# Optimization experiments

Measured on AMD Instinct MI355X. Metric: run time of the kernel, lower is better.

The kernel has to match this reference:

```python
import jax, jax.numpy as jnp
import numpy as np

A = 81          # agents / zones (9x9 grid)
DMAX = 5        # max neighborhood size (self + 4-neighbors)
NGLOB = 48      # global obs block width
HID = 128
B = 16384
LN_EPS = 1e-12  # tf.contrib.layers.layer_norm epsilon
BN_EPS = 1e-3   # tf.contrib.layers.batch_norm epsilon
NEG = -1e30


def _grid_adjacency():
    side = 9
    idx = np.zeros((A, DMAX), np.int32)
    mask = np.zeros((A, DMAX), bool)
    for i in range(A):
        r, c = divmod(i, side)
        nb = [i]
        for dr, dc in ((-1, 0), (1, 0), (0, -1), (0, 1)):
            rr, cc = r + dr, c + dc
            if 0 <= rr < side and 0 <= cc < side:
                nb.append(rr * side + cc)
        idx[i, :len(nb)] = nb
        mask[i, :len(nb)] = True
    return jnp.asarray(idx), jnp.asarray(mask)


def setup_inputs() -> dict:
    key = jax.random.key(0)
    ks = jax.random.split(key, 8)
    neigh_idx, neigh_mask = _grid_adjacency()
    in_dim = 2 * DMAX + NGLOB  # padded local obs width (58)
    s = 0.05
    return {
        "obs": jax.random.normal(ks[0], (B, 210), jnp.float32),
        "neigh_idx": neigh_idx,
        "neigh_mask": neigh_mask,
        "W1": jax.random.normal(ks[1], (A, in_dim, HID), jnp.float32) * s,
        "b1": jnp.zeros((A, HID), jnp.float32),
        "ln1_g": jnp.ones((A, HID), jnp.float32),
        "ln1_b": jnp.zeros((A, HID), jnp.float32),
        "bn1_b": jnp.zeros((A, HID), jnp.float32),
        "W2": jax.random.normal(ks[2], (A, HID, HID), jnp.float32) * s,
        "b2": jnp.zeros((A, HID), jnp.float32),
        "ln2_g": jnp.ones((A, HID), jnp.float32),
        "ln2_b": jnp.zeros((A, HID), jnp.float32),
        "bn2_b": jnp.zeros((A, HID), jnp.float32),
        "Wout": jax.random.normal(ks[3], (A, HID, DMAX), jnp.float32) * s,
        "bout": jnp.zeros((A, DMAX), jnp.float32),
    }


def _layer_norm(x, g, b):
    mu = jnp.mean(x, axis=-1, keepdims=True)
    var = jnp.mean(jnp.square(x - mu), axis=-1, keepdims=True)
    return (x - mu) * jax.lax.rsqrt(var + LN_EPS) * g[:, None, :] + b[:, None, :]


def _batch_norm(x, beta):
    # training-mode batch norm over the batch axis (axis=1), center only (scale=False)
    mu = jnp.mean(x, axis=1, keepdims=True)
    var = jnp.mean(jnp.square(x - mu), axis=1, keepdims=True)
    return (x - mu) * jax.lax.rsqrt(var + BN_EPS) + beta[:, None, :]


def reference(obs, neigh_idx, neigh_mask, W1, b1, ln1_g, ln1_b, bn1_b,
              W2, b2, ln2_g, ln2_b, bn2_b, Wout, bout):
    m = neigh_mask[:, None, :].astype(obs.dtype)          # [A,1,DMAX]
    g1 = obs[:, NGLOB + neigh_idx].transpose(1, 0, 2)      # [A,B,DMAX] zone block 1
    g2 = obs[:, NGLOB + 81 + neigh_idx].transpose(1, 0, 2)  # [A,B,DMAX] zone block 2
    glob = jnp.broadcast_to(obs[None, :, :NGLOB], (A, obs.shape[0], NGLOB))
    x = jnp.concatenate([g1 * m, g2 * m, glob], axis=-1)   # [A,B,58] (padded slots zeroed)

    h = jnp.einsum('abi,aio->abo', x, W1) + b1[:, None, :]
    h = jax.nn.relu(_batch_norm(_layer_norm(h, ln1_g, ln1_b), bn1_b))
    h = jnp.einsum('abi,aio->abo', h, W2) + b2[:, None, :]
    h = jax.nn.relu(_batch_norm(_layer_norm(h, ln2_g, ln2_b), bn2_b))

    logits = jnp.einsum('abi,aid->abd', h, Wout) + bout[:, None, :]  # [A,B,DMAX]
    logits = jnp.where(neigh_mask[:, None, :], logits, NEG)
    p = jax.nn.softmax(logits, axis=-1) * m                # masked softmax over valid neighbors

    oh = jax.nn.one_hot(neigh_idx, A, dtype=p.dtype)       # [A,DMAX,81] scatter map
    out = jnp.einsum('abd,adn->abn', p, oh)                # scatter into fixed 81-vector
    return out.transpose(1, 0, 2)                          # [B,A,81]
```

## Files before the change

kernel.cpp:

```cpp
#include <hip/hip_runtime.h>
#include <stdint.h>
#include <stddef.h>

#define N_AG 81
#define HID 128
#define TROWS 128

typedef __bf16 bf16x8 __attribute__((ext_vector_type(8)));
typedef float f32x4 __attribute__((ext_vector_type(4)));
typedef uint32_t u32v4 __attribute__((ext_vector_type(4)));
typedef uint32_t u32v2 __attribute__((ext_vector_type(2)));

#define PB1 0
#define PLG1 128
#define PLB1 256
#define PBN1 384
#define PMU1 512
#define PRS1 640
#define PB2 768
#define PLG2 896
#define PLB2 1024
#define PBN2 1152
#define PMU2 1280
#define PRS2 1408

__device__ __forceinline__ unsigned short f2bf(float f) {
  uint32_t u = __builtin_bit_cast(uint32_t, f);
  u += 0x7fffu + ((u >> 16) & 1u);
  return (unsigned short)(u >> 16);
}

__device__ __forceinline__ f32x4 f4z() { f32x4 v; v[0]=0.f; v[1]=0.f; v[2]=0.f; v[3]=0.f; return v; }

__device__ __forceinline__ bf16x8 ld_frag(const uint8_t* p) {
  u32v4 v = *(const u32v4*)p;
  return __builtin_bit_cast(bf16x8, v);
}

__device__ __forceinline__ f32x4 mfma16(bf16x8 a, bf16x8 b, f32x4 c) {
  return __builtin_amdgcn_mfma_f32_16x16x32_bf16(a, b, c, 0, 0, 0);
}

__device__ __forceinline__ void bias_ln(f32x4 (&acc)[8][2], const float* s_par,
                                        int PB, int PG, int PBb, int g) {
  #pragma unroll
  for (int mf = 0; mf < 8; ++mf) {
    #pragma unroll
    for (int rg = 0; rg < 4; ++rg) {
      float bo = s_par[PB + 16 * mf + 4 * g + rg];
      acc[mf][0][rg] += bo;
      acc[mf][1][rg] += bo;
    }
  }
  #pragma unroll
  for (int nf = 0; nf < 2; ++nf) {
    float s = 0.f;
    #pragma unroll
    for (int mf = 0; mf < 8; ++mf) {
      #pragma unroll
      for (int rg = 0; rg < 4; ++rg) s += acc[mf][nf][rg];
    }
    s += __shfl_xor(s, 16);
    s += __shfl_xor(s, 32);
    float mu = s * (1.f / 128.f);
    float qs = 0.f;
    #pragma unroll
    for (int mf = 0; mf < 8; ++mf) {
      #pragma unroll
      for (int rg = 0; rg < 4; ++rg) { float d = acc[mf][nf][rg] - mu; qs += d * d; }
    }
    qs += __shfl_xor(qs, 16);
    qs += __shfl_xor(qs, 32);
    float rstd = rsqrtf(qs * (1.f / 128.f) + 1e-12f);
    #pragma unroll
    for (int mf = 0; mf < 8; ++mf) {
      #pragma unroll
      for (int rg = 0; rg < 4; ++rg) {
        int o = 16 * mf + 4 * g + rg;
        acc[mf][nf][rg] = (acc[mf][nf][rg] - mu) * rstd * s_par[PG + o] + s_par[PBb + o];
      }
    }
  }
}

__device__ __forceinline__ void stats_wave(const f32x4 (&acc)[8][2],
                                           float (&s_red)[2][4][128],
                                           int wv, int g, int q) {
  #pragma unroll
  for (int mf = 0; mf < 8; ++mf) {
    #pragma unroll
    for (int rg = 0; rg < 4; ++rg) {
      float s = acc[mf][0][rg] + acc[mf][1][rg];
      float qq = acc[mf][0][rg] * acc[mf][0][rg] + acc[mf][1][rg] * acc[mf][1][rg];
      s += __shfl_xor(s, 1); s += __shfl_xor(s, 2); s += __shfl_xor(s, 4); s += __shfl_xor(s, 8);
      qq += __shfl_xor(qq, 1); qq += __shfl_xor(qq, 2); qq += __shfl_xor(qq, 4); qq += __shfl_xor(qq, 8);
      if (q == 0) {
        int o = 16 * mf + 4 * g + rg;
        s_red[0][wv][o] = s;
        s_red[1][wv][o] = qq;
      }
    }
  }
}

__global__ void prep_weights(const float* __restrict__ W1, const float* __restrict__ W2,
                             uint8_t* __restrict__ w1img, uint8_t* __restrict__ w2img) {
  const int a = blockIdx.x, t = threadIdx.x;
  for (int i = t; i < 128 * 64; i += 256) {
    int o = i & 127, kk = i >> 7;
    float v;
    if (kk < 48)      v = W1[((size_t)a * 58 + (10 + kk)) * 128 + o];
    else if (kk < 58) v = W1[((size_t)a * 58 + (kk - 48)) * 128 + o];
    else              v = 0.f;
    uint32_t cb = 2u * kk;
    uint32_t phys = o * 128 + (((cb & ~15u) ^ (((uint32_t)o & 7u) << 4)) | (cb & 15u));
    *(unsigned short*)(w1img + (size_t)a * 16384 + phys) = f2bf(v);
  }
  for (int i = t; i < 128 * 128; i += 256) {
    int o = i & 127, kk = i >> 7;
    float v = W2[((size_t)a * 128 + kk) * 128 + o];
    uint32_t cb = 2u * kk;
    uint32_t phys = o * 256 + (((cb & ~15u) ^ (((uint32_t)o & 7u) << 4)) | (cb & 15u));
    *(unsigned short*)(w2img + (size_t)a * 32768 + phys) = f2bf(v);
  }
}

__global__ void prep_obs(const float* __restrict__ obs, uint8_t* __restrict__ globimg) {
  const int row = blockIdx.x * 256 + threadIdx.x;
  if (row >= 16384) return;
  const float* orow = obs + (size_t)row * 210;
  uint8_t* dst = globimg + (size_t)row * 96;
  #pragma unroll
  for (int c = 0; c < 6; ++c) {
    u32v4 pk;
    #pragma unroll
    for (int e = 0; e < 4; ++e) {
      float va = orow[8 * c + 2 * e];
      float vb = orow[8 * c + 2 * e + 1];
      pk[e] = (uint32_t)f2bf(va) | ((uint32_t)f2bf(vb) << 16);
    }
    *(u32v4*)(dst + 16 * c) = pk;
  }
}

__global__ void reduce_stats(const float* __restrict__ partS, const float* __restrict__ partQ,
                             float* __restrict__ mu, float* __restrict__ rs) {
  const int a = blockIdx.x, c = threadIdx.x;
  float S = 0.f, Q = 0.f;
  for (int tb = 0; tb < 32; ++tb) {
    S += partS[((size_t)a * 32 + tb) * HID + c];
    Q += partQ[((size_t)a * 32 + tb) * HID + c];
  }
  float m = S * (1.f / 16384.f);
  float v = Q * (1.f / 16384.f) - m * m;
  mu[a * HID + c] = m;
  rs[a * HID + c] = rsqrtf(v + 1e-3f);
}

template <int PASS>
__launch_bounds__(256, (PASS == 1) ? 4 : 2)
__global__ void pass_kernel(
    const float* __restrict__ obs, const int* __restrict__ nidx,
    const float* __restrict__ b1, const float* __restrict__ ln1g,
    const float* __restrict__ ln1b, const float* __restrict__ bnb1,
    const float* __restrict__ b2, const float* __restrict__ ln2g,
    const float* __restrict__ ln2b, const float* __restrict__ bnb2,
    const float* __restrict__ wout, const float* __restrict__ boutp,
    const uint8_t* __restrict__ w1img, const uint8_t* __restrict__ w2img,
    const uint8_t* __restrict__ globimg,
    const float* __restrict__ mu1, const float* __restrict__ rs1,
    const float* __restrict__ mu2, const float* __restrict__ rs2,
    float* __restrict__ partS, float* __restrict__ partQ,
    float* __restrict__ out) {
  constexpr int MAINSZ = (PASS == 1) ? 32768 : 65536;
  constexpr int PARSZ = (PASS == 1) ? 384 : 1536;
  __shared__ __align__(16) uint8_t s_main[MAINSZ];
  __shared__ float s_par[PARSZ];
  __shared__ float s_red[2][4][128];
  __shared__ float s_wout[(PASS == 3) ? 640 : 4];
  __shared__ float s_bout[8];

  const int t = threadIdx.x;
  const int wv = t >> 6, l = t & 63, g = l >> 4, q = l & 15;

  const int a = blockIdx.x >> 5;
  const int sub = blockIdx.x & 31;
  const int tile0 = sub * 4;

  const int r9 = a / 9, c9 = a - 9 * r9;
  const int deg = 1 + (r9 > 0) + (r9 < 8) + (c9 > 0) + (c9 < 8);
  int nid[5];
  #pragma unroll
  for (int d = 0; d < 5; ++d) nid[d] = nidx[a * 5 + d];

  if (t < HID) {
    s_par[PB1 + t] = b1[a * HID + t];
    s_par[PLG1 + t] = ln1g[a * HID + t];
    s_par[PLB1 + t] = ln1b[a * HID + t];
    if constexpr (PASS >= 2) {
      s_par[PBN1 + t] = bnb1[a * HID + t];
      s_par[PMU1 + t] = mu1[a * HID + t];
      s_par[PRS1 + t] = rs1[a * HID + t];
      s_par[PB2 + t] = b2[a * HID + t];
      s_par[PLG2 + t] = ln2g[a * HID + t];
      s_par[PLB2 + t] = ln2b[a * HID + t];
    }
    if constexpr (PASS == 3) {
      s_par[PBN2 + t] = bnb2[a * HID + t];
      s_par[PMU2 + t] = mu2[a * HID + t];
      s_par[PRS2 + t] = rs2[a * HID + t];
      #pragma unroll
      for (int d = 0; d < 5; ++d) s_wout[t * 5 + d] = wout[(a * HID + t) * 5 + d];
    }
  }
  if constexpr (PASS == 3) {
    if (t < 5) s_bout[t] = boutp[a * 5 + t];
  }

  float Sacc = 0.f, Qacc = 0.f;
  const uint8_t* w1src = w1img + (size_t)a * 16384;
  const uint8_t* w2src = w2img + (size_t)a * 32768;

  for (int tt = 0; tt < 4; ++tt) {
    const int tile = tile0 + tt;

    {
      const uint8_t* src = globimg + (size_t)tile * (128 * 96);
      #pragma unroll
      for (int j = 0; j < 3; ++j) {
        int u = 3 * t + j;
        int r = u / 6, c = u - 6 * r;
        u32v4 v = *(const u32v4*)(src + (size_t)u * 16);
        *(u32v4*)(s_main + r * 128 + (((uint32_t)c ^ ((uint32_t)r & 7u)) << 4)) = v;
      }
    }
    if (PASS != 1 || tt == 0) {
      #pragma unroll
      for (int i = 0; i < 4; ++i) {
        int idx = t + 256 * i;
        ((u32v4*)(s_main + 16384))[idx] = ((const u32v4*)w1src)[idx];
      }
    }
    if constexpr (PASS >= 2) {
      if (PASS == 3 || tt == 0) {
        #pragma unroll
        for (int i = 0; i < 8; ++i) {
          int idx = t + 256 * i;
          ((u32v4*)(s_main + 32768))[idx] = ((const u32v4*)w2src)[idx];
        }
      }
    }
    if (t < 128) {
      const int r = t;
      const float* orow = obs + (size_t)(tile * TROWS + r) * 210;
      unsigned short us[10];
      #pragma unroll
      for (int d = 0; d < 5; ++d) {
        us[d] = (d < deg) ? f2bf(orow[48 + nid[d]]) : (unsigned short)0;
        us[5 + d] = (d < deg) ? f2bf(orow[129 + nid[d]]) : (unsigned short)0;
      }
      u32v4 c6, c7;
      c6[0] = (uint32_t)us[0] | ((uint32_t)us[1] << 16);
      c6[1] = (uint32_t)us[2] | ((uint32_t)us[3] << 16);
      c6[2] = (uint32_t)us[4] | ((uint32_t)us[5] << 16);
      c6[3] = (uint32_t)us[6] | ((uint32_t)us[7] << 16);
      c7[0] = (uint32_t)us[8] | ((uint32_t)us[9] << 16);
      c7[1] = 0u; c7[2] = 0u; c7[3] = 0u;
      *(u32v4*)(s_main + r * 128 + ((6u ^ ((uint32_t)r & 7u)) << 4)) = c6;
      *(u32v4*)(s_main + r * 128 + ((7u ^ ((uint32_t)r & 7u)) << 4)) = c7;
    }
    __syncthreads();

    f32x4 acc1[8][2];
    #pragma unroll
    for (int mf = 0; mf < 8; ++mf) { acc1[mf][0] = f4z(); acc1[mf][1] = f4z(); }
    {
      const uint8_t* sx = s_main;
      const uint8_t* sw1 = s_main + 16384;
      const int rb = 32 * wv;
      #pragma unroll
      for (int ks = 0; ks < 2; ++ks) {
        bf16x8 bfr[2];
        #pragma unroll
        for (int nf = 0; nf < 2; ++nf) {
          uint32_t r = rb + 16 * nf + q;
          uint32_t cb = ((uint32_t)(64 * ks + 16 * g)) ^ ((r & 7u) << 4);
          bfr[nf] = ld_frag(sx + r * 128 + cb);
        }
        #pragma unroll
        for (int mf = 0; mf < 8; ++mf) {
          uint32_t r = 16 * mf + q;
          uint32_t cb = ((uint32_t)(64 * ks + 16 * g)) ^ ((r & 7u) << 4);
          bf16x8 af = ld_frag(sw1 + r * 128 + cb);
          acc1[mf][0] = mfma16(af, bfr[0], acc1[mf][0]);
          acc1[mf][1] = mfma16(af, bfr[1], acc1[mf][1]);
        }
      }
    }

    bias_ln(acc1, s_par, PB1, PLG1, PLB1, g);

    if constexpr (PASS == 1) {
      stats_wave(acc1, s_red, wv, g, q);
      __syncthreads();
      if (t < HID) {
        Sacc += s_red[0][0][t] + s_red[0][1][t] + s_red[0][2][t] + s_red[0][3][t];
        Qacc += s_red[1][0][t] + s_red[1][1][t] + s_red[1][2][t] + s_red[1][3][t];
      }
    } else {
      __syncthreads();
      #pragma unroll
      for (int mf = 0; mf < 8; ++mf) {
        #pragma unroll
        for (int nf = 0; nf < 2; ++nf) {
          unsigned short us[4];
          #pragma unroll
          for (int rg = 0; rg < 4; ++rg) {
            int o = 16 * mf + 4 * g + rg;
            float z = (acc1[mf][nf][rg] - s_par[PMU1 + o]) * s_par[PRS1 + o] + s_par[PBN1 + o];
            us[rg] = f2bf(fmaxf(z, 0.f));
          }
          uint32_t b_ = 32 * wv + 16 * nf + q;
          uint32_t cb = 2u * (16 * mf + 4 * g);
          uint32_t phys = b_ * 256 + (((cb & ~15u) ^ ((b_ & 7u) << 4)) | (cb & 15u));
          u32v2 pk;
          pk[0] = (uint32_t)us[0] | ((uint32_t)us[1] << 16);
          pk[1] = (uint32_t)us[2] | ((uint32_t)us[3] << 16);
          *(u32v2*)(s_main + phys) = pk;
        }
      }
      __syncthreads();

      f32x4 acc2[8][2];
      #pragma unroll
      for (int mf = 0; mf < 8; ++mf) { acc2[mf][0] = f4z(); acc2[mf][1] = f4z(); }
      {
        const uint8_t* sh1 = s_main;
        const uint8_t* sw2 = s_main + 32768;
        #pragma unroll
        for (int ks2 = 0; ks2 < 4; ++ks2) {
          bf16x8 bfr[2];
          #pragma unroll
          for (int nf = 0; nf < 2; ++nf) {
            uint32_t r = 32 * wv + 16 * nf + q;
            uint32_t cb = ((uint32_t)(64 * ks2 + 16 * g)) ^ ((r & 7u) << 4);
            bfr[nf] = ld_frag(sh1 + r * 256 + cb);
          }
          #pragma unroll
          for (int mf = 0; mf < 8; ++mf) {
            uint32_t r = 16 * mf + q;
            uint32_t cb = ((uint32_t)(64 * ks2 + 16 * g)) ^ ((r & 7u) << 4);
            bf16x8 af = ld_frag(sw2 + r * 256 + cb);
            acc2[mf][0] = mfma16(af, bfr[0], acc2[mf][0]);
            acc2[mf][1] = mfma16(af, bfr[1], acc2[mf][1]);
          }
        }
      }

      bias_ln(acc2, s_par, PB2, PLG2, PLB2, g);

      if constexpr (PASS == 2) {
        stats_wave(acc2, s_red, wv, g, q);
        __syncthreads();
        if (t < HID) {
          Sacc += s_red[0][0][t] + s_red[0][1][t] + s_red[0][2][t] + s_red[0][3][t];
          Qacc += s_red[1][0][t] + s_red[1][1][t] + s_red[1][2][t] + s_red[1][3][t];
        }
      }

      if constexpr (PASS == 3) {
        float lg[2][5];
        #pragma unroll
        for (int nf = 0; nf < 2; ++nf) {
          #pragma unroll
          for (int d = 0; d < 5; ++d) lg[nf][d] = 0.f;
        }
        #pragma unroll
        for (int mf = 0; mf < 8; ++mf) {
          #pragma unroll
          for (int rg = 0; rg < 4; ++rg) {
            int o = 16 * mf + 4 * g + rg;
            float m2 = s_par[PMU2 + o], r2 = s_par[PRS2 + o], bb2 = s_par[PBN2 + o];
            float h0 = fmaxf((acc2[mf][0][rg] - m2) * r2 + bb2, 0.f);
            float h1v = fmaxf((acc2[mf][1][rg] - m2) * r2 + bb2, 0.f);
            #pragma unroll
            for (int d = 0; d < 5; ++d) {
              float wvv = s_wout[o * 5 + d];
              lg[0][d] += h0 * wvv;
              lg[1][d] += h1v * wvv;
            }
          }
        }
        #pragma unroll
        for (int nf = 0; nf < 2; ++nf) {
          #pragma unroll
          for (int d = 0; d < 5; ++d) {
            float v = lg[nf][d];
            v += __shfl_xor(v, 16);
            v += __shfl_xor(v, 32);
            lg[nf][d] = v + s_bout[d];
          }
        }
        float p[2][5];
        #pragma unroll
        for (int nf = 0; nf < 2; ++nf) {
          float mx = lg[nf][0];
          #pragma unroll
          for (int d = 1; d < 5; ++d)
            if (d < deg) mx = fmaxf(mx, lg[nf][d]);
          float den = 0.f;
          #pragma unroll
          for (int d = 0; d < 5; ++d) {
            float e = (d < deg) ? __expf(lg[nf][d] - mx) : 0.f;
            p[nf][d] = e;
            den += e;
          }
          float inv = 1.f / den;
          #pragma unroll
          for (int d = 0; d < 5; ++d) p[nf][d] *= inv;
        }

        __syncthreads();
        float* s_out = (float*)s_main;
        #pragma unroll
        for (int i = 0; i < 11; ++i) {
          int idx = t + 256 * i;
          if (idx < 2688) {
            u32v4 z; z[0] = 0u; z[1] = 0u; z[2] = 0u; z[3] = 0u;
            ((u32v4*)s_out)[idx] = z;
          }
        }
        __syncthreads();
        #pragma unroll
        for (int d = 0; d < 5; ++d) {
          bool writer = (d < 4) ? (g == d) : (g == 0);
          if (writer && d < deg) {
            s_out[(32 * wv + q) * 84 + nid[d]] = p[0][d];
            s_out[(32 * wv + 16 + q) * 84 + nid[d]] = p[1][d];
          }
        }
        __syncthreads();
        const size_t obase = (size_t)(tile * TROWS) * 6561 + (size_t)a * 81;
        for (int i = t; i < 128 * 81; i += 256) {
          int r = i / 81;
          int n = i - r * 81;
          out[obase + (size_t)r * 6561 + n] = s_out[r * 84 + n];
        }
        __syncthreads();
      }
    }
  }

  if constexpr (PASS != 3) {
    if (t < HID) {
      partS[((size_t)a * 32 + sub) * HID + t] = Sacc;
      partQ[((size_t)a * 32 + sub) * HID + t] = Qacc;
    }
  }
}

extern "C" void kernel_launch(void* const* d_in, const int* in_sizes, int n_in,
                              void* d_out, int out_size, void* d_ws, size_t ws_size,
                              hipStream_t stream) {
  const float* obs = (const float*)d_in[0];
  const int* nidx = (const int*)d_in[1];
  const float* W1 = (const float*)d_in[3];
  const float* b1 = (const float*)d_in[4];
  const float* ln1g = (const float*)d_in[5];
  const float* ln1b = (const float*)d_in[6];
  const float* bnb1 = (const float*)d_in[7];
  const float* W2 = (const float*)d_in[8];
  const float* b2 = (const float*)d_in[9];
  const float* ln2g = (const float*)d_in[10];
  const float* ln2b = (const float*)d_in[11];
  const float* bnb2 = (const float*)d_in[12];
  const float* Wout = (const float*)d_in[13];
  const float* bout = (const float*)d_in[14];
  float* out = (float*)d_out;
  uint8_t* ws = (uint8_t*)d_ws;

  uint8_t* w1img = ws;
  uint8_t* w2img = ws + 1327104;
  uint8_t* globimg = ws + 3981312;
  float* partS1 = (float*)(ws + 5554176);
  float* partQ1 = (float*)(ws + 6881280);
  float* partS2 = (float*)(ws + 8208384);
  float* partQ2 = (float*)(ws + 9535488);
  float* mu1 = (float*)(ws + 10862592);
  float* rs1 = (float*)(ws + 10904064);
  float* mu2 = (float*)(ws + 10945536);
  float* rs2 = (float*)(ws + 10987008);

  prep_weights<<<N_AG, 256, 0, stream>>>(W1, W2, w1img, w2img);
  prep_obs<<<64, 256, 0, stream>>>(obs, globimg);

  pass_kernel<1><<<N_AG * 32, 256, 0, stream>>>(
      obs, nidx, b1, ln1g, ln1b, bnb1, b2, ln2g, ln2b, bnb2, Wout, bout,
      w1img, w2img, globimg, mu1, rs1, mu2, rs2, partS1, partQ1, out);
  reduce_stats<<<N_AG, 128, 0, stream>>>(partS1, partQ1, mu1, rs1);

  pass_kernel<2><<<N_AG * 32, 256, 0, stream>>>(
      obs, nidx, b1, ln1g, ln1b, bnb1, b2, ln2g, ln2b, bnb2, Wout, bout,
      w1img, w2img, globimg, mu1, rs1, mu2, rs2, partS2, partQ2, out);
  reduce_stats<<<N_AG, 128, 0, stream>>>(partS2, partQ2, mu2, rs2);

  pass_kernel<3><<<N_AG * 32, 256, 0, stream>>>(
      obs, nidx, b1, ln1g, ln1b, bnb1, b2, ln2g, ln2b, bnb2, Wout, bout,
      w1img, w2img, globimg, mu1, rs1, mu2, rs2, partS1, partQ1, out);
}
```

Before: 891.2 us.

## Materialize LN outputs in bf16 workspace instead of recomputing layers per pass

The three-pass recompute scheme, where later passes rerun layer-1 (and layer-2) GEMMs, is replaced. Each pass now writes its layer-normalized activations as a bf16 tile image to workspace, and the next pass reads them back, applying batch norm on the fly. BN statistics are accumulated with global atomics instead of per-block partials. Wout moves to an MFMA path, the output scatter writes rows directly with vector stores, and passes run in agent chunks sized to the workspace. This trades GEMM recomputation for extra global-memory traffic and adds bf16 rounding of intermediate activations, which could affect accuracy.

```diff
diff --git a/kernel.cpp b/kernel.cpp
--- a/kernel.cpp
+++ b/kernel.cpp
@@ -3,31 +3,19 @@
 #include <stddef.h>
 
 #define N_AG 81
-#define HID 128
-#define TROWS 128
 
 typedef __bf16 bf16x8 __attribute__((ext_vector_type(8)));
 typedef float f32x4 __attribute__((ext_vector_type(4)));
+typedef f32x4 __attribute__((aligned(4))) f32x4u;
 typedef uint32_t u32v4 __attribute__((ext_vector_type(4)));
 typedef uint32_t u32v2 __attribute__((ext_vector_type(2)));
 
-#define PB1 0
-#define PLG1 128
-#define PLB1 256
-#define PBN1 384
-#define PMU1 512
-#define PRS1 640
-#define PB2 768
-#define PLG2 896
-#define PLB2 1024
-#define PBN2 1152
-#define PMU2 1280
-#define PRS2 1408
-
-__device__ __forceinline__ unsigned short f2bf(float f) {
-  uint32_t u = __builtin_bit_cast(uint32_t, f);
-  u += 0x7fffu + ((u >> 16) & 1u);
-  return (unsigned short)(u >> 16);
+#define PB 0
+#define PG 128
+#define PBT 256
+
+__device__ __forceinline__ unsigned short b2u(__bf16 h) {
+  return __builtin_bit_cast(unsigned short, h);
 }
 
 __device__ __forceinline__ f32x4 f4z() { f32x4 v; v[0]=0.f; v[1]=0.f; v[2]=0.f; v[3]=0.f; return v; }
@@ -41,70 +29,103 @@
   return __builtin_amdgcn_mfma_f32_16x16x32_bf16(a, b, c, 0, 0, 0);
 }
 
-__device__ __forceinline__ void bias_ln(f32x4 (&acc)[8][2], const float* s_par,
-                                        int PB, int PG, int PBb, int g) {
-  #pragma unroll
-  for (int mf = 0; mf < 8; ++mf) {
-    #pragma unroll
-    for (int rg = 0; rg < 4; ++rg) {
-      float bo = s_par[PB + 16 * mf + 4 * g + rg];
-      acc[mf][0][rg] += bo;
-      acc[mf][1][rg] += bo;
-    }
-  }
+__device__ __forceinline__ float wave16_sum(float v) {
+  v += __builtin_bit_cast(float, __builtin_amdgcn_update_dpp(0, __builtin_bit_cast(int, v), 0xB1, 0xF, 0xF, true));
+  v += __builtin_bit_cast(float, __builtin_amdgcn_update_dpp(0, __builtin_bit_cast(int, v), 0x4E, 0xF, 0xF, true));
+  v += __builtin_bit_cast(float, __builtin_amdgcn_update_dpp(0, __builtin_bit_cast(int, v), 0x141, 0xF, 0xF, true));
+  v += __builtin_bit_cast(float, __builtin_amdgcn_update_dpp(0, __builtin_bit_cast(int, v), 0x140, 0xF, 0xF, true));
+  return v;
+}
+
+__device__ __forceinline__ bf16x8 mk_frag(const unsigned short (&us)[8]) {
+  u32v4 pk;
+  pk[0] = (uint32_t)us[0] | ((uint32_t)us[1] << 16);
+  pk[1] = (uint32_t)us[2] | ((uint32_t)us[3] << 16);
+  pk[2] = (uint32_t)us[4] | ((uint32_t)us[5] << 16);
+  pk[3] = (uint32_t)us[6] | ((uint32_t)us[7] << 16);
+  return __builtin_bit_cast(bf16x8, pk);
+}
+
+__device__ __forceinline__ bf16x8 bn_frag(u32v2 lo, u32v2 hi, const f32x4 (&cf)[4]) {
+  bf16x8 r;
+  #pragma unroll
+  for (int j = 0; j < 8; ++j) {
+    uint32_t wrd = (j < 4) ? lo[(j >> 1) & 1] : hi[(j >> 1) & 1];
+    uint32_t us = (j & 1) ? (wrd >> 16) : (wrd & 0xffffu);
+    float f = __builtin_bit_cast(float, us << 16);
+    float h = fmaf(f, cf[j >> 1][(j & 1) * 2], cf[j >> 1][(j & 1) * 2 + 1]);
+    r[j] = (__bf16)fmaxf(h, 0.f);
+  }
+  return r;
+}
+
+__device__ __forceinline__ void bias_ln(f32x4 (&acc)[8][2], const float* s_par, int g) {
   #pragma unroll
   for (int nf = 0; nf < 2; ++nf) {
-    float s = 0.f;
+    float s = 0.f, qs = 0.f;
     #pragma unroll
     for (int mf = 0; mf < 8; ++mf) {
       #pragma unroll
-      for (int rg = 0; rg < 4; ++rg) s += acc[mf][nf][rg];
-    }
-    s += __shfl_xor(s, 16);
-    s += __shfl_xor(s, 32);
+      for (int rg = 0; rg < 4; ++rg) {
+        float tv = acc[mf][nf][rg] + s_par[PB + 16 * mf + 4 * g + rg];
+        acc[mf][nf][rg] = tv;
+        s += tv;
+        qs = fmaf(tv, tv, qs);
+      }
+    }
+    s += __shfl_xor(s, 16);  s += __shfl_xor(s, 32);
+    qs += __shfl_xor(qs, 16); qs += __shfl_xor(qs, 32);
     float mu = s * (1.f / 128.f);
-    float qs = 0.f;
-    #pragma unroll
-    for (int mf = 0; mf < 8; ++mf) {
-      #pragma unroll
-      for (int rg = 0; rg < 4; ++rg) { float d = acc[mf][nf][rg] - mu; qs += d * d; }
-    }
-    qs += __shfl_xor(qs, 16);
-    qs += __shfl_xor(qs, 32);
-    float rstd = rsqrtf(qs * (1.f / 128.f) + 1e-12f);
+    float var = qs * (1.f / 128.f) - mu * mu;
+    float rstd = rsqrtf(var + 1e-12f);
     #pragma unroll
     for (int mf = 0; mf < 8; ++mf) {
       #pragma unroll
       for (int rg = 0; rg < 4; ++rg) {
         int o = 16 * mf + 4 * g + rg;
-        acc[mf][nf][rg] = (acc[mf][nf][rg] - mu) * rstd * s_par[PG + o] + s_par[PBb + o];
-      }
-    }
-  }
-}
-
-__device__ __forceinline__ void stats_wave(const f32x4 (&acc)[8][2],
-                                           float (&s_red)[2][4][128],
-                                           int wv, int g, int q) {
+        acc[mf][nf][rg] = (acc[mf][nf][rg] - mu) * rstd * s_par[PG + o] + s_par[PBT + o];
+      }
+    }
+  }
+}
+
+__device__ __forceinline__ void stats_atomic(const f32x4 (&acc)[8][2], float* pS, float* pQ,
+                                             int g, int q) {
   #pragma unroll
   for (int mf = 0; mf < 8; ++mf) {
     #pragma unroll
     for (int rg = 0; rg < 4; ++rg) {
-      float s = acc[mf][0][rg] + acc[mf][1][rg];
-      float qq = acc[mf][0][rg] * acc[mf][0][rg] + acc[mf][1][rg] * acc[mf][1][rg];
-      s += __shfl_xor(s, 1); s += __shfl_xor(s, 2); s += __shfl_xor(s, 4); s += __shfl_xor(s, 8);
-      qq += __shfl_xor(qq, 1); qq += __shfl_xor(qq, 2); qq += __shfl_xor(qq, 4); qq += __shfl_xor(qq, 8);
+      float a0v = acc[mf][0][rg], a1v = acc[mf][1][rg];
+      float s = a0v + a1v;
+      float qq = fmaf(a0v, a0v, a1v * a1v);
+      s = wave16_sum(s);
+      qq = wave16_sum(qq);
       if (q == 0) {
         int o = 16 * mf + 4 * g + rg;
-        s_red[0][wv][o] = s;
-        s_red[1][wv][o] = qq;
-      }
+        atomicAdd(pS + o, s);
+        atomicAdd(pQ + o, qq);
+      }
+    }
+  }
+}
+
+__device__ __forceinline__ void store_ytile(const f32x4 (&acc)[8][2], uint8_t* ytile, int t) {
+  #pragma unroll
+  for (int mf = 0; mf < 8; ++mf) {
+    #pragma unroll
+    for (int nf = 0; nf < 2; ++nf) {
+      u32v2 pk;
+      pk[0] = (uint32_t)b2u((__bf16)acc[mf][nf][0]) | ((uint32_t)b2u((__bf16)acc[mf][nf][1]) << 16);
+      pk[1] = (uint32_t)b2u((__bf16)acc[mf][nf][2]) | ((uint32_t)b2u((__bf16)acc[mf][nf][3]) << 16);
+      *(u32v2*)(ytile + ((((uint32_t)mf << 1) + nf) << 11) + t * 8) = pk;
     }
   }
 }
 
 __global__ void prep_weights(const float* __restrict__ W1, const float* __restrict__ W2,
-                             uint8_t* __restrict__ w1img, uint8_t* __restrict__ w2img) {
+                             const float* __restrict__ Wout,
+                             uint8_t* __restrict__ w1img, uint8_t* __restrict__ w2img,
+                             uint8_t* __restrict__ woimg) {
   const int a = blockIdx.x, t = threadIdx.x;
   for (int i = t; i < 128 * 64; i += 256) {
     int o = i & 127, kk = i >> 7;
@@ -114,14 +135,21 @@
     else              v = 0.f;
     uint32_t cb = 2u * kk;
     uint32_t phys = o * 128 + (((cb & ~15u) ^ (((uint32_t)o & 7u) << 4)) | (cb & 15u));
-    *(unsigned short*)(w1img + (size_t)a * 16384 + phys) = f2bf(v);
+    *(unsigned short*)(w1img + (size_t)a * 16384 + phys) = b2u((__bf16)v);
   }
   for (int i = t; i < 128 * 128; i += 256) {
     int o = i & 127, kk = i >> 7;
     float v = W2[((size_t)a * 128 + kk) * 128 + o];
     uint32_t cb = 2u * kk;
     uint32_t phys = o * 256 + (((cb & ~15u) ^ (((uint32_t)o & 7u) << 4)) | (cb & 15u));
-    *(unsigned short*)(w2img + (size_t)a * 32768 + phys) = f2bf(v);
+    *(unsigned short*)(w2img + (size_t)a * 32768 + phys) = b2u((__bf16)v);
+  }
+  for (int i = t; i < 16 * 128; i += 256) {
+    int k = i & 127, d = i >> 7;
+    float v = (d < 5) ? Wout[((size_t)a * 128 + k) * 5 + d] : 0.f;
+    uint32_t cb = 2u * k;
+    uint32_t phys = d * 256 + (((cb & ~15u) ^ (((uint32_t)d & 7u) << 4)) | (cb & 15u));
+    *(unsigned short*)(woimg + (size_t)a * 4096 + phys) = b2u((__bf16)v);
   }
 }
 
@@ -135,326 +163,295 @@
     u32v4 pk;
     #pragma unroll
     for (int e = 0; e < 4; ++e) {
-      float va = orow[8 * c + 2 * e];
-      float vb = orow[8 * c + 2 * e + 1];
-      pk[e] = (uint32_t)f2bf(va) | ((uint32_t)f2bf(vb) << 16);
+      pk[e] = (uint32_t)b2u((__bf16)orow[8 * c + 2 * e]) |
+              ((uint32_t)b2u((__bf16)orow[8 * c + 2 * e + 1]) << 16);
     }
     *(u32v4*)(dst + 16 * c) = pk;
   }
 }
 
-__global__ void reduce_stats(const float* __restrict__ partS, const float* __restrict__ partQ,
-                             float* __restrict__ mu, float* __restrict__ rs) {
-  const int a = blockIdx.x, c = threadIdx.x;
-  float S = 0.f, Q = 0.f;
-  for (int tb = 0; tb < 32; ++tb) {
-    S += partS[((size_t)a * 32 + tb) * HID + c];
-    Q += partQ[((size_t)a * 32 + tb) * HID + c];
-  }
-  float m = S * (1.f / 16384.f);
-  float v = Q * (1.f / 16384.f) - m * m;
-  mu[a * HID + c] = m;
-  rs[a * HID + c] = rsqrtf(v + 1e-3f);
-}
-
-template <int PASS>
-__launch_bounds__(256, (PASS == 1) ? 4 : 2)
-__global__ void pass_kernel(
-    const float* __restrict__ obs, const int* __restrict__ nidx,
-    const float* __restrict__ b1, const float* __restrict__ ln1g,
-    const float* __restrict__ ln1b, const float* __restrict__ bnb1,
-    const float* __restrict__ b2, const float* __restrict__ ln2g,
-    const float* __restrict__ ln2b, const float* __restrict__ bnb2,
-    const float* __restrict__ wout, const float* __restrict__ boutp,
-    const uint8_t* __restrict__ w1img, const uint8_t* __restrict__ w2img,
-    const uint8_t* __restrict__ globimg,
-    const float* __restrict__ mu1, const float* __restrict__ rs1,
-    const float* __restrict__ mu2, const float* __restrict__ rs2,
-    float* __restrict__ partS, float* __restrict__ partQ,
-    float* __restrict__ out) {
-  constexpr int MAINSZ = (PASS == 1) ? 32768 : 65536;
-  constexpr int PARSZ = (PASS == 1) ? 384 : 1536;
-  __shared__ __align__(16) uint8_t s_main[MAINSZ];
-  __shared__ float s_par[PARSZ];
-  __shared__ float s_red[2][4][128];
-  __shared__ float s_wout[(PASS == 3) ? 640 : 4];
-  __shared__ float s_bout[8];
+__global__ void reduce_bn(const float* __restrict__ S, const float* __restrict__ Q,
+                          const float* __restrict__ beta, float2* __restrict__ bn, int a0) {
+  const int a = a0 + blockIdx.x, k = threadIdx.x;
+  float mu = S[a * 128 + k] * (1.f / 16384.f);
+  float var = Q[a * 128 + k] * (1.f / 16384.f) - mu * mu;
+  float rs = rsqrtf(var + 1e-3f);
+  bn[a * 128 + k] = make_float2(rs, beta[a * 128 + k] - mu * rs);
+}
+
+__launch_bounds__(256, 4)
+__global__ void pass1_kernel(const float* __restrict__ obs, const int* __restrict__ nidx,
+                             const float* __restrict__ b1, const float* __restrict__ ln1g,
+                             const float* __restrict__ ln1b,
+                             const uint8_t* __restrict__ w1img,
+                             const uint8_t* __restrict__ globimg,
+                             float* __restrict__ statS, float* __restrict__ statQ,
+                             uint8_t* __restrict__ yimg, int a0) {
+  __shared__ __align__(16) uint8_t s_w1[16384];
+  __shared__ float s_par[384];
 
   const int t = threadIdx.x;
   const int wv = t >> 6, l = t & 63, g = l >> 4, q = l & 15;
-
-  const int a = blockIdx.x >> 5;
+  const int a = a0 + (blockIdx.x >> 5);
   const int sub = blockIdx.x & 31;
-  const int tile0 = sub * 4;
 
   const int r9 = a / 9, c9 = a - 9 * r9;
   const int deg = 1 + (r9 > 0) + (r9 < 8) + (c9 > 0) + (c9 < 8);
   int nid[5];
   #pragma unroll
-  for (int d = 0; d < 5; ++d) nid[d] = nidx[a * 5 + d];
-
-  if (t < HID) {
-    s_par[PB1 + t] = b1[a * HID + t];
-    s_par[PLG1 + t] = ln1g[a * HID + t];
-    s_par[PLB1 + t] = ln1b[a * HID + t];
-    if constexpr (PASS >= 2) {
-      s_par[PBN1 + t] = bnb1[a * HID + t];
-      s_par[PMU1 + t] = mu1[a * HID + t];
-      s_par[PRS1 + t] = rs1[a * HID + t];
-      s_par[PB2 + t] = b2[a * HID + t];
-      s_par[PLG2 + t] = ln2g[a * HID + t];
-      s_par[PLB2 + t] = ln2b[a * HID + t];
-    }
-    if constexpr (PASS == 3) {
-      s_par[PBN2 + t] = bnb2[a * HID + t];
-      s_par[PMU2 + t] = mu2[a * HID + t];
-      s_par[PRS2 + t] = rs2[a * HID + t];
-      #pragma unroll
-      for (int d = 0; d < 5; ++d) s_wout[t * 5 + d] = wout[(a * HID + t) * 5 + d];
-    }
-  }
-  if constexpr (PASS == 3) {
-    if (t < 5) s_bout[t] = boutp[a * 5 + t];
-  }
-
-  float Sacc = 0.f, Qacc = 0.f;
+  for (int d = 0; d < 5; ++d) nid[d] = __builtin_amdgcn_readfirstlane(nidx[a * 5 + d]);
+
   const uint8_t* w1src = w1img + (size_t)a * 16384;
-  const uint8_t* w2src = w2img + (size_t)a * 32768;
+  #pragma unroll
+  for (int i = 0; i < 4; ++i) ((u32v4*)s_w1)[t + 256 * i] = ((const u32v4*)w1src)[t + 256 * i];
+  if (t < 128) {
+    s_par[PB + t] = b1[a * 128 + t];
+    s_par[PG + t] = ln1g[a * 128 + t];
+    s_par[PBT + t] = ln1b[a * 128 + t];
+  }
+  __syncthreads();
+
+  float* pS = statS + a * 128;
+  float* pQ = statQ + a * 128;
 
   for (int tt = 0; tt < 4; ++tt) {
-    const int tile = tile0 + tt;
-
-    {
-      const uint8_t* src = globimg + (size_t)tile * (128 * 96);
-      #pragma unroll
-      for (int j = 0; j < 3; ++j) {
-        int u = 3 * t + j;
-        int r = u / 6, c = u - 6 * r;
-        u32v4 v = *(const u32v4*)(src + (size_t)u * 16);
-        *(u32v4*)(s_main + r * 128 + (((uint32_t)c ^ ((uint32_t)r & 7u)) << 4)) = v;
-      }
-    }
-    if (PASS != 1 || tt == 0) {
-      #pragma unroll
-      for (int i = 0; i < 4; ++i) {
-        int idx = t + 256 * i;
-        ((u32v4*)(s_main + 16384))[idx] = ((const u32v4*)w1src)[idx];
-      }
-    }
-    if constexpr (PASS >= 2) {
-      if (PASS == 3 || tt == 0) {
-        #pragma unroll
-        for (int i = 0; i < 8; ++i) {
-          int idx = t + 256 * i;
-          ((u32v4*)(s_main + 32768))[idx] = ((const u32v4*)w2src)[idx];
-        }
-      }
-    }
-    if (t < 128) {
-      const int r = t;
-      const float* orow = obs + (size_t)(tile * TROWS + r) * 210;
-      unsigned short us[10];
-      #pragma unroll
-      for (int d = 0; d < 5; ++d) {
-        us[d] = (d < deg) ? f2bf(orow[48 + nid[d]]) : (unsigned short)0;
-        us[5 + d] = (d < deg) ? f2bf(orow[129 + nid[d]]) : (unsigned short)0;
-      }
-      u32v4 c6, c7;
-      c6[0] = (uint32_t)us[0] | ((uint32_t)us[1] << 16);
-      c6[1] = (uint32_t)us[2] | ((uint32_t)us[3] << 16);
-      c6[2] = (uint32_t)us[4] | ((uint32_t)us[5] << 16);
-      c6[3] = (uint32_t)us[6] | ((uint32_t)us[7] << 16);
-      c7[0] = (uint32_t)us[8] | ((uint32_t)us[9] << 16);
-      c7[1] = 0u; c7[2] = 0u; c7[3] = 0u;
-      *(u32v4*)(s_main + r * 128 + ((6u ^ ((uint32_t)r & 7u)) << 4)) = c6;
-      *(u32v4*)(s_main + r * 128 + ((7u ^ ((uint32_t)r & 7u)) << 4)) = c7;
-    }
-    __syncthreads();
-
-    f32x4 acc1[8][2];
-    #pragma unroll
-    for (int mf = 0; mf < 8; ++mf) { acc1[mf][0] = f4z(); acc1[mf][1] = f4z(); }
-    {
-      const uint8_t* sx = s_main;
-      const uint8_t* sw1 = s_main + 16384;
-      const int rb = 32 * wv;
-      #pragma unroll
-      for (int ks = 0; ks < 2; ++ks) {
-        bf16x8 bfr[2];
-        #pragma unroll
-        for (int nf = 0; nf < 2; ++nf) {
-          uint32_t r = rb + 16 * nf + q;
-          uint32_t cb = ((uint32_t)(64 * ks + 16 * g)) ^ ((r & 7u) << 4);
-          bfr[nf] = ld_frag(sx + r * 128 + cb);
-        }
-        #pragma unroll
-        for (int mf = 0; mf < 8; ++mf) {
-          uint32_t r = 16 * mf + q;
-          uint32_t cb = ((uint32_t)(64 * ks + 16 * g)) ^ ((r & 7u) << 4);
-          bf16x8 af = ld_frag(sw1 + r * 128 + cb);
-          acc1[mf][0] = mfma16(af, bfr[0], acc1[mf][0]);
-          acc1[mf][1] = mfma16(af, bfr[1], acc1[mf][1]);
-        }
-      }
-    }
-
-    bias_ln(acc1, s_par, PB1, PLG1, PLB1, g);
-
-    if constexpr (PASS == 1) {
-      stats_wave(acc1, s_red, wv, g, q);
-      __syncthreads();
-      if (t < HID) {
-        Sacc += s_red[0][0][t] + s_red[0][1][t] + s_red[0][2][t] + s_red[0][3][t];
-        Qacc += s_red[1][0][t] + s_red[1][1][t] + s_red[1][2][t] + s_red[1][3][t];
-      }
-    } else {
-      __syncthreads();
-      #pragma unroll
-      for (int mf = 0; mf < 8; ++mf) {
-        #pragma unroll
-        for (int nf = 0; nf < 2; ++nf) {
-          unsigned short us[4];
-          #pragma unroll
-          for (int rg = 0; rg < 4; ++rg) {
-            int o = 16 * mf + 4 * g + rg;
-            float z = (acc1[mf][nf][rg] - s_par[PMU1 + o]) * s_par[PRS1 + o] + s_par[PBN1 + o];
-            us[rg] = f2bf(fmaxf(z, 0.f));
-          }
-          uint32_t b_ = 32 * wv + 16 * nf + q;
-          uint32_t cb = 2u * (16 * mf + 4 * g);
-          uint32_t phys = b_ * 256 + (((cb & ~15u) ^ ((b_ & 7u) << 4)) | (cb & 15u));
-          u32v2 pk;
-          pk[0] = (uint32_t)us[0] | ((uint32_t)us[1] << 16);
-          pk[1] = (uint32_t)us[2] | ((uint32_t)us[3] << 16);
-          *(u32v2*)(s_main + phys) = pk;
-        }
-      }
-      __syncthreads();
-
-      f32x4 acc2[8][2];
-      #pragma unroll
-      for (int mf = 0; mf < 8; ++mf) { acc2[mf][0] = f4z(); acc2[mf][1] = f4z(); }
-      {
-        const uint8_t* sh1 = s_main;
-        const uint8_t* sw2 = s_main + 32768;
-        #pragma unroll
-        for (int ks2 = 0; ks2 < 4; ++ks2) {
-          bf16x8 bfr[2];
-          #pragma unroll
-          for (int nf = 0; nf < 2; ++nf) {
-            uint32_t r = 32 * wv + 16 * nf + q;
-            uint32_t cb = ((uint32_t)(64 * ks2 + 16 * g)) ^ ((r & 7u) << 4);
-            bfr[nf] = ld_frag(sh1 + r * 256 + cb);
-          }
-          #pragma unroll
-          for (int mf = 0; mf < 8; ++mf) {
-            uint32_t r = 16 * mf + q;
-            uint32_t cb = ((uint32_t)(64 * ks2 + 16 * g)) ^ ((r & 7u) << 4);
-            bf16x8 af = ld_frag(sw2 + r * 256 + cb);
-            acc2[mf][0] = mfma16(af, bfr[0], acc2[mf][0]);
-            acc2[mf][1] = mfma16(af, bfr[1], acc2[mf][1]);
-          }
-        }
-      }
-
-      bias_ln(acc2, s_par, PB2, PLG2, PLB2, g);
-
-      if constexpr (PASS == 2) {
-        stats_wave(acc2, s_red, wv, g, q);
-        __syncthreads();
-        if (t < HID) {
-          Sacc += s_red[0][0][t] + s_red[0][1][t] + s_red[0][2][t] + s_red[0][3][t];
-          Qacc += s_red[1][0][t] + s_red[1][1][t] + s_red[1][2][t] + s_red[1][3][t];
-        }
-      }
-
-      if constexpr (PASS == 3) {
-        float lg[2][5];
-        #pragma unroll
-        for (int nf = 0; nf < 2; ++nf) {
-          #pragma unroll
-          for (int d = 0; d < 5; ++d) lg[nf][d] = 0.f;
-        }
-        #pragma unroll
-        for (int mf = 0; mf < 8; ++mf) {
-          #pragma unroll
-          for (int rg = 0; rg < 4; ++rg) {
-            int o = 16 * mf + 4 * g + rg;
-            float m2 = s_par[PMU2 + o], r2 = s_par[PRS2 + o], bb2 = s_par[PBN2 + o];
-            float h0 = fmaxf((acc2[mf][0][rg] - m2) * r2 + bb2, 0.f);
-            float h1v = fmaxf((acc2[mf][1][rg] - m2) * r2 + bb2, 0.f);
+    const int tile = sub * 4 + tt;
+
+    bf16x8 bfr[2][2];
+    #pragma unroll
+    for (int ks = 0; ks < 2; ++ks) {
+      #pragma unroll
+      for (int nf = 0; nf < 2; ++nf) {
+        const int brow = tile * 128 + 32 * wv + 16 * nf + q;
+        if (ks == 1 && g >= 2) {
+          const float* orow = obs + (size_t)brow * 210;
+          unsigned short us[8];
+          if (g == 2) {
             #pragma unroll
-            for (int d = 0; d < 5; ++d) {
-              float wvv = s_wout[o * 5 + d];
-              lg[0][d] += h0 * wvv;
-              lg[1][d] += h1v * wvv;
+            for (int e = 0; e < 8; ++e) {
+              float v;
+              if (e < 5) v = (e < deg) ? orow[48 + nid[e]] : 0.f;
+              else       v = ((e - 5) < deg) ? orow[129 + nid[e - 5]] : 0.f;
+              us[e] = b2u((__bf16)v);
+            }
+          } else {
+            #pragma unroll
+            for (int e = 0; e < 8; ++e) {
+              float v = (e < 2 && (3 + e) < deg) ? orow[129 + nid[3 + e]] : 0.f;
+              us[e] = b2u((__bf16)v);
             }
           }
+          bfr[ks][nf] = mk_frag(us);
+        } else {
+          bfr[ks][nf] = *(const bf16x8*)(globimg + (size_t)brow * 96 + (32 * ks + 8 * g) * 2);
         }
+      }
+    }
+
+    f32x4 acc[8][2];
+    #pragma unroll
+    for (int mf = 0; mf < 8; ++mf) { acc[mf][0] = f4z(); acc[mf][1] = f4z(); }
+    #pragma unroll
+    for (int ks = 0; ks < 2; ++ks) {
+      #pragma unroll
+      for (int mf = 0; mf < 8; ++mf) {
+        uint32_t r = 16 * mf + q;
+        uint32_t cb = ((uint32_t)(64 * ks + 16 * g)) ^ ((r & 7u) << 4);
+        bf16x8 af = ld_frag(s_w1 + r * 128 + cb);
+        acc[mf][0] = mfma16(af, bfr[ks][0], acc[mf][0]);
+        acc[mf][1] = mfma16(af, bfr[ks][1], acc[mf][1]);
+      }
+    }
+
+    bias_ln(acc, s_par, g);
+    stats_atomic(acc, pS, pQ, g, q);
+
+    uint8_t* ytile = yimg + ((((size_t)(a - a0)) * 128 + tile) << 15);
+    store_ytile(acc, ytile, t);
+  }
+}
+
+__launch_bounds__(256, 4)
+__global__ void pass2_kernel(const float* __restrict__ b2, const float* __restrict__ ln2g,
+                             const float* __restrict__ ln2b,
+                             const uint8_t* __restrict__ w2img,
+                             const float2* __restrict__ bn1,
+                             float* __restrict__ statS, float* __restrict__ statQ,
+                             uint8_t* __restrict__ yimg, int a0) {
+  __shared__ __align__(16) uint8_t s_w2[32768];
+  __shared__ float s_par[384];
+  __shared__ __align__(16) float2 s_bnc[128];
+
+  const int t = threadIdx.x;
+  const int wv = t >> 6, l = t & 63, g = l >> 4, q = l & 15;
+  const int a = a0 + (blockIdx.x >> 5);
+  const int sub = blockIdx.x & 31;
+
+  const uint8_t* w2src = w2img + (size_t)a * 32768;
+  #pragma unroll
+  for (int i = 0; i < 8; ++i) ((u32v4*)s_w2)[t + 256 * i] = ((const u32v4*)w2src)[t + 256 * i];
+  if (t < 128) {
+    s_par[PB + t] = b2[a * 128 + t];
+    s_par[PG + t] = ln2g[a * 128 + t];
+    s_par[PBT + t] = ln2b[a * 128 + t];
+    s_bnc[t] = bn1[a * 128 + t];
+  }
+  __syncthreads();
+
+  float* pS = statS + a * 128;
+  float* pQ = statQ + a * 128;
+
+  for (int tt = 0; tt < 4; ++tt) {
+    const int tile = sub * 4 + tt;
+    uint8_t* ytile = yimg + ((((size_t)(a - a0)) * 128 + tile) << 15);
+
+    f32x4 acc[8][2];
+    #pragma unroll
+    for (int mf = 0; mf < 8; ++mf) { acc[mf][0] = f4z(); acc[mf][1] = f4z(); }
+
+    #pragma unroll
+    for (int ks2 = 0; ks2 < 4; ++ks2) {
+      const int k0 = 32 * ks2 + 8 * g;
+      f32x4 cf[4];
+      #pragma unroll
+      for (int i = 0; i < 4; ++i)
+        cf[i] = *(const f32x4*)((const uint8_t*)s_bnc + k0 * 8 + 16 * i);
+      const int mfp = 2 * ks2 + (g >> 1);
+      bf16x8 bfr[2];
+      #pragma unroll
+      for (int nf = 0; nf < 2; ++nf) {
+        const uint8_t* p0 = ytile + ((((uint32_t)mfp << 1) + nf) << 11) +
+                            (64 * wv + 32 * (g & 1) + q) * 8;
+        u32v2 lo = *(const u32v2*)p0;
+        u32v2 hi = *(const u32v2*)(p0 + 128);
+        bfr[nf] = bn_frag(lo, hi, cf);
+      }
+      #pragma unroll
+      for (int mf = 0; mf < 8; ++mf) {
+        uint32_t r = 16 * mf + q;
+        uint32_t cb = ((uint32_t)(64 * ks2 + 16 * g)) ^ ((r & 7u) << 4);
+        bf16x8 af = ld_frag(s_w2 + r * 256 + cb);
+        acc[mf][0] = mfma16(af, bfr[0], acc[mf][0]);
+        acc[mf][1] = mfma16(af, bfr[1], acc[mf][1]);
+      }
+    }
+
+    bias_ln(acc, s_par, g);
+    stats_atomic(acc, pS, pQ, g, q);
+    store_ytile(acc, ytile, t);
+  }
+}
+
+__launch_bounds__(256, 4)
+__global__ void pass3_kernel(const int* __restrict__ nidx, const float* __restrict__ boutp,
+                             const uint8_t* __restrict__ woimg,
+                             const float2* __restrict__ bn2,
+                             const uint8_t* __restrict__ yimg,
+                             float* __restrict__ out, int a0) {
+  __shared__ __align__(16) uint8_t s_wo[4096];
+  __shared__ __align__(16) float2 s_bnc[128];
+  __shared__ float s_bout[16];
+
+  const int t = threadIdx.x;
+  const int wv = t >> 6, l = t & 63, g = l >> 4, q = l & 15;
+  const int a = a0 + (blockIdx.x >> 5);
+  const int sub = blockIdx.x & 31;
+
+  const int r9 = a / 9, c9 = a - 9 * r9;
+  const int deg = 1 + (r9 > 0) + (r9 < 8) + (c9 > 0) + (c9 < 8);
+  int nid[5];
+  #pragma unroll
+  for (int d = 0; d < 5; ++d) nid[d] = __builtin_amdgcn_readfirstlane(nidx[a * 5 + d]);
+
+  ((u32v4*)s_wo)[t] = ((const u32v4*)(woimg + (size_t)a * 4096))[t];
+  if (t < 128) s_bnc[t] = bn2[a * 128 + t];
+  if (t < 16) s_bout[t] = (t < 5) ? boutp[a * 5 + t] : 0.f;
+  __syncthreads();
+
+  bf16x8 afr[4];
+  #pragma unroll
+  for (int ks2 = 0; ks2 < 4; ++ks2) {
+    uint32_t cb = ((uint32_t)(64 * ks2 + 16 * g)) ^ (((uint32_t)q & 7u) << 4);
+    afr[ks2] = ld_frag(s_wo + q * 256 + cb);
+  }
+
+  for (int tt = 0; tt < 4; ++tt) {
+    const int tile = sub * 4 + tt;
+    const uint8_t* ytile = yimg + ((((size_t)(a - a0)) * 128 + tile) << 15);
+
+    f32x4 accd[2];
+    accd[0] = f4z(); accd[1] = f4z();
+
+    #pragma unroll
+    for (int ks2 = 0; ks2 < 4; ++ks2) {
+      const int k0 = 32 * ks2 + 8 * g;
+      f32x4 cf[4];
+      #pragma unroll
+      for (int i = 0; i < 4; ++i)
+        cf[i] = *(const f32x4*)((const uint8_t*)s_bnc + k0 * 8 + 16 * i);
+      const int mfp = 2 * ks2 + (g >> 1);
+      #pragma unroll
+      for (int nf = 0; nf < 2; ++nf) {
+        const uint8_t* p0 = ytile + ((((uint32_t)mfp << 1) + nf) << 11) +
+                            (64 * wv + 32 * (g & 1) + q) * 8;
+        u32v2 lo = *(const u32v2*)p0;
+        u32v2 hi = *(const u32v2*)(p0 + 128);
+        accd[nf] = mfma16(afr[ks2], bn_frag(lo, hi, cf), accd[nf]);
+      }
+    }
+
+    #pragma unroll
+    for (int nf = 0; nf < 2; ++nf) {
+      #pragma unroll
+      for (int rg = 0; rg < 4; ++rg) accd[nf][rg] += s_bout[4 * g + rg];
+    }
+    float d4[2];
+    d4[0] = __shfl_xor(accd[0][0], 16);
+    d4[1] = __shfl_xor(accd[1][0], 16);
+
+    float p[2][5];
+    #pragma unroll
+    for (int nf = 0; nf < 2; ++nf) {
+      float v[5] = {accd[nf][0], accd[nf][1], accd[nf][2], accd[nf][3], d4[nf]};
+      float mx = v[0];
+      #pragma unroll
+      for (int d = 1; d < 5; ++d)
+        if (d < deg) mx = fmaxf(mx, v[d]);
+      float den = 0.f;
+      #pragma unroll
+      for (int d = 0; d < 5; ++d) {
+        float e = (d < deg) ? __expf(v[d] - mx) : 0.f;
+        p[nf][d] = e;
+        den += e;
+      }
+      float inv = 1.f / den;
+      #pragma unroll
+      for (int d = 0; d < 5; ++d) p[nf][d] *= inv;
+    }
+
+    float p5[5];
+    #pragma unroll
+    for (int d = 0; d < 5; ++d) {
+      float pr = __shfl_xor(p[1][d], 32);
+      p5[d] = (g == 0) ? p[0][d] : pr;
+    }
+
+    if (g == 0 || g == 2) {
+      const int brow = tile * 128 + 32 * wv + ((g == 2) ? 16 : 0) + q;
+      float* orow = out + ((size_t)brow * 81 + (size_t)a) * 81;
+      #pragma unroll
+      for (int c = 0; c < 20; ++c) {
+        f32x4u v = {0.f, 0.f, 0.f, 0.f};
         #pragma unroll
-        for (int nf = 0; nf < 2; ++nf) {
-          #pragma unroll
-          for (int d = 0; d < 5; ++d) {
-            float v = lg[nf][d];
-            v += __shfl_xor(v, 16);
-            v += __shfl_xor(v, 32);
-            lg[nf][d] = v + s_bout[d];
-          }
-        }
-        float p[2][5];
-        #pragma unroll
-        for (int nf = 0; nf < 2; ++nf) {
-          float mx = lg[nf][0];
-          #pragma unroll
-          for (int d = 1; d < 5; ++d)
-            if (d < deg) mx = fmaxf(mx, lg[nf][d]);
-          float den = 0.f;
-          #pragma unroll
-          for (int d = 0; d < 5; ++d) {
-            float e = (d < deg) ? __expf(lg[nf][d] - mx) : 0.f;
-            p[nf][d] = e;
-            den += e;
-          }
-          float inv = 1.f / den;
-          #pragma unroll
-          for (int d = 0; d < 5; ++d) p[nf][d] *= inv;
-        }
-
-        __syncthreads();
-        float* s_out = (float*)s_main;
-        #pragma unroll
-        for (int i = 0; i < 11; ++i) {
-          int idx = t + 256 * i;
-          if (idx < 2688) {
-            u32v4 z; z[0] = 0u; z[1] = 0u; z[2] = 0u; z[3] = 0u;
-            ((u32v4*)s_out)[idx] = z;
-          }
-        }
-        __syncthreads();
-        #pragma unroll
-        for (int d = 0; d < 5; ++d) {
-          bool writer = (d < 4) ? (g == d) : (g == 0);
-          if (writer && d < deg) {
-            s_out[(32 * wv + q) * 84 + nid[d]] = p[0][d];
-            s_out[(32 * wv + 16 + q) * 84 + nid[d]] = p[1][d];
-          }
-        }
-        __syncthreads();
-        const size_t obase = (size_t)(tile * TROWS) * 6561 + (size_t)a * 81;
-        for (int i = t; i < 128 * 81; i += 256) {
-          int r = i / 81;
-          int n = i - r * 81;
-          out[obase + (size_t)r * 6561 + n] = s_out[r * 84 + n];
-        }
-        __syncthreads();
-      }
-    }
-  }
-
-  if constexpr (PASS != 3) {
-    if (t < HID) {
-      partS[((size_t)a * 32 + sub) * HID + t] = Sacc;
-      partQ[((size_t)a * 32 + sub) * HID + t] = Qacc;
+        for (int d = 0; d < 5; ++d)
+          if (d < deg && (nid[d] >> 2) == c) v[nid[d] & 3] = p5[d];
+        *(f32x4u*)(orow + 4 * c) = v;
+      }
+      float vl = 0.f;
+      #pragma unroll
+      for (int d = 0; d < 5; ++d)
+        if (d < deg && nid[d] == 80) vl = p5[d];
+      orow[80] = vl;
     }
   }
 }
@@ -462,6 +459,7 @@
 extern "C" void kernel_launch(void* const* d_in, const int* in_sizes, int n_in,
                               void* d_out, int out_size, void* d_ws, size_t ws_size,
                               hipStream_t stream) {
+  (void)in_sizes; (void)n_in; (void)out_size;
   const float* obs = (const float*)d_in[0];
   const int* nidx = (const int*)d_in[1];
   const float* W1 = (const float*)d_in[3];
@@ -479,32 +477,36 @@
   float* out = (float*)d_out;
   uint8_t* ws = (uint8_t*)d_ws;
 
-  uint8_t* w1img = ws;
-  uint8_t* w2img = ws + 1327104;
-  uint8_t* globimg = ws + 3981312;
-  float* partS1 = (float*)(ws + 5554176);
-  float* partQ1 = (float*)(ws + 6881280);
-  float* partS2 = (float*)(ws + 8208384);
-  float* partQ2 = (float*)(ws + 9535488);
-  float* mu1 = (float*)(ws + 10862592);
-  float* rs1 = (float*)(ws + 10904064);
-  float* mu2 = (float*)(ws + 10945536);
-  float* rs2 = (float*)(ws + 10987008);
-
-  prep_weights<<<N_AG, 256, 0, stream>>>(W1, W2, w1img, w2img);
+  uint8_t* w1img   = ws;
+  uint8_t* w2img   = ws + 1327104;
+  uint8_t* woimg   = ws + 3981312;
+  uint8_t* globimg = ws + 4313088;
+  float* statS1 = (float*)(ws + 5885952);
+  float* statQ1 = (float*)(ws + 5927424);
+  float* statS2 = (float*)(ws + 5968896);
+  float* statQ2 = (float*)(ws + 6010368);
+  float2* bn1 = (float2*)(ws + 6051840);
+  float2* bn2 = (float2*)(ws + 6134784);
+  uint8_t* yimg = ws + 6217728;
+
+  size_t ybytes = (ws_size > 6217728) ? ws_size - 6217728 : 0;
+  int na = (int)(ybytes / 4194304);
+  if (na < 1) na = 1;
+  if (na > N_AG) na = N_AG;
+
+  prep_weights<<<N_AG, 256, 0, stream>>>(W1, W2, Wout, w1img, w2img, woimg);
   prep_obs<<<64, 256, 0, stream>>>(obs, globimg);
-
-  pass_kernel<1><<<N_AG * 32, 256, 0, stream>>>(
-      obs, nidx, b1, ln1g, ln1b, bnb1, b2, ln2g, ln2b, bnb2, Wout, bout,
-      w1img, w2img, globimg, mu1, rs1, mu2, rs2, partS1, partQ1, out);
-  reduce_stats<<<N_AG, 128, 0, stream>>>(partS1, partQ1, mu1, rs1);
-
-  pass_kernel<2><<<N_AG * 32, 256, 0, stream>>>(
-      obs, nidx, b1, ln1g, ln1b, bnb1, b2, ln2g, ln2b, bnb2, Wout, bout,
-      w1img, w2img, globimg, mu1, rs1, mu2, rs2, partS2, partQ2, out);
-  reduce_stats<<<N_AG, 128, 0, stream>>>(partS2, partQ2, mu2, rs2);
-
-  pass_kernel<3><<<N_AG * 32, 256, 0, stream>>>(
-      obs, nidx, b1, ln1g, ln1b, bnb1, b2, ln2g, ln2b, bnb2, Wout, bout,
-      w1img, w2img, globimg, mu1, rs1, mu2, rs2, partS1, partQ1, out);
-}
+  hipMemsetAsync(statS1, 0, 4 * 41472, stream);
+
+  for (int a0 = 0; a0 < N_AG; a0 += na) {
+    int nc = N_AG - a0;
+    if (nc > na) nc = na;
+    pass1_kernel<<<nc * 32, 256, 0, stream>>>(obs, nidx, b1, ln1g, ln1b, w1img, globimg,
+                                              statS1, statQ1, yimg, a0);
+    reduce_bn<<<nc, 128, 0, stream>>>(statS1, statQ1, bnb1, bn1, a0);
+    pass2_kernel<<<nc * 32, 256, 0, stream>>>(b2, ln2g, ln2b, w2img, bn1,
+                                              statS2, statQ2, yimg, a0);
+    reduce_bn<<<nc, 128, 0, stream>>>(statS2, statQ2, bnb2, bn2, a0);
+    pass3_kernel<<<nc * 32, 256, 0, stream>>>(nidx, bout, woimg, bn2, yimg, out, a0);
+  }
+}
```

Result: slower. 2.690 ms (+201.8%).
